# Performance work log

Measured on AMD Instinct MI355X. Metric: run time of the kernel, lower is better.

## Reference

```python
import jax, jax.numpy as jnp
import numpy as np

NUM_HEADS = 8
HEAD_DIM = 128
MAX_RES = 224.0


def rope_embed(feat_shape, dim, max_res=MAX_RES):
    # timm pixel_freq_bands: 2**linspace(0, log2(max_res)-1, dim//4) * pi
    num_bands = dim // 4
    bands = (2.0 ** jnp.linspace(0.0, float(np.log2(max_res)) - 1.0, num_bands)) * jnp.pi
    # pixel coords in [-1, 1] per spatial dim
    coords = [jnp.linspace(-1.0, 1.0, s) for s in feat_shape]
    grid = jnp.stack(jnp.meshgrid(*coords, indexing='ij'), axis=-1)[..., None]  # [H,W,2,1]
    pos = grid * bands  # [H,W,2,num_bands]
    n = int(np.prod(feat_shape))
    sin = jnp.repeat(jnp.sin(pos).reshape(n, -1), 2, axis=-1)  # [n, dim]
    cos = jnp.repeat(jnp.cos(pos).reshape(n, -1), 2, axis=-1)  # [n, dim]
    return sin, cos


def _rot(x):
    # interleaved rotate-half: (x0,x1,x2,x3,...) -> (-x1,x0,-x3,x2,...)
    return jnp.stack([-x[..., 1::2], x[..., ::2]], axis=-1).reshape(x.shape)


def setup_inputs() -> dict:
    key = jax.random.key(0)
    k1, k2, k3, k4 = jax.random.split(key, 4)
    C, E = 1024, 1024
    x = jax.random.normal(k1, (64, C, 16, 16), dtype=jnp.float32)
    qkv_w = jax.random.normal(k2, (3 * E, C), dtype=jnp.float32) * (C ** -0.5)
    qkv_b = jnp.zeros((3 * E,), dtype=jnp.float32)
    proj_w = jax.random.normal(k3, (E, E), dtype=jnp.float32) * (E ** -0.5)
    proj_b = jax.random.normal(k4, (E,), dtype=jnp.float32) * 0.02
    return {"x": x, "qkv_w": qkv_w, "qkv_b": qkv_b, "proj_w": proj_w, "proj_b": proj_b}


def reference(x, qkv_w, qkv_b, proj_w, proj_b):
    B, C, H, W = x.shape
    n = H * W
    scale = HEAD_DIM ** -0.5
    sin_emb, cos_emb = rope_embed((H, W), HEAD_DIM)  # [n, head_dim]

    t = x.reshape(B, C, n).transpose(0, 2, 1)                      # [B, n, C]
    t = jnp.concatenate([t.mean(axis=1, keepdims=True), t], axis=1)  # [B, n+1, C]

    qkv = t @ qkv_w.T + qkv_b                                      # [B, n+1, 3E]
    qkv = qkv.reshape(B, n + 1, 3, NUM_HEADS, HEAD_DIM).transpose(2, 0, 3, 1, 4)
    q, k, v = qkv[0], qkv[1], qkv[2]                               # [B, h, n+1, d]

    def apply_rope(z):
        zc, zs = z[:, :, :1], z[:, :, 1:]
        zs = zs * cos_emb + _rot(zs) * sin_emb
        return jnp.concatenate([zc, zs], axis=2)

    q = apply_rope(q)
    k = apply_rope(k)

    attn = jax.nn.softmax(jnp.einsum('bhqd,bhkd->bhqk', q, k) * scale, axis=-1)
    out = jnp.einsum('bhqk,bhkd->bhqd', attn, v)
    out = out.transpose(0, 2, 1, 3).reshape(B, n + 1, -1)           # [B, n+1, E]
    out = out @ proj_w.T + proj_b
    return out[:, 0]
```

## Files before the change

kernel.cpp:

```cpp
#include <hip/hip_runtime.h>
#include <math.h>

#define PI_F 3.14159265358979323846f
#define KSTEP 0.21959209425992272f

using bf16x8 = __attribute__((ext_vector_type(8))) short;
using f32x4 = __attribute__((ext_vector_type(4))) float;
using u16x8 = __attribute__((ext_vector_type(8))) unsigned short;

static __device__ __forceinline__ float wave_reduce_sum(float v) {
#pragma unroll
  for (int off = 32; off; off >>= 1) v += __shfl_down(v, off);
  return v;
}

static __device__ __forceinline__ unsigned short f2bf(float f) {
  unsigned u = __float_as_uint(f);
  return (unsigned short)((u + 0x7fffu + ((u >> 16) & 1u)) >> 16);
}

static __device__ __forceinline__ float bf2f(unsigned short s) {
  return __uint_as_float(((unsigned)s) << 16);
}

static __device__ __forceinline__ void gload_lds16(const void* g, void* l) {
  __builtin_amdgcn_global_load_lds((const __attribute__((address_space(1))) unsigned int*)g,
                                   (__attribute__((address_space(3))) unsigned int*)l, 16, 0, 0);
}

__global__ __launch_bounds__(256) void prep_kernel(const float* __restrict__ x,
                                                   const float* __restrict__ qkv_w,
                                                   const float* __restrict__ qkv_b,
                                                   unsigned short* __restrict__ xt,
                                                   float* __restrict__ t_mean,
                                                   unsigned short* __restrict__ wkT,
                                                   float2* __restrict__ sc) {
  const int bid = blockIdx.x;
  const int t = threadIdx.x;
  __shared__ float tile[64 * 33];
  __shared__ float tl2[64 * 65];
  if (bid < 1024) {
    const int ct = bid & 15, b = bid >> 4;
    const int cl = t >> 2, pq = (t & 3) * 8;
    const int pl = t >> 3, cq = (t & 7) * 8;
    float sum = 0.0f;
    const float* xrow = x + ((size_t)(b * 1024 + ct * 64 + cl) * 256) + pq;
    unsigned short* xtb = xt + (size_t)b * 262144 + ct * 64;
    for (int pt = 0; pt < 8; ++pt) {
      const float4 v0 = *reinterpret_cast<const float4*>(xrow + pt * 32);
      const float4 v1 = *reinterpret_cast<const float4*>(xrow + pt * 32 + 4);
      tile[cl * 33 + pq + 0] = v0.x; tile[cl * 33 + pq + 1] = v0.y;
      tile[cl * 33 + pq + 2] = v0.z; tile[cl * 33 + pq + 3] = v0.w;
      tile[cl * 33 + pq + 4] = v1.x; tile[cl * 33 + pq + 5] = v1.y;
      tile[cl * 33 + pq + 6] = v1.z; tile[cl * 33 + pq + 7] = v1.w;
      sum += (v0.x + v0.y) + (v0.z + v0.w) + (v1.x + v1.y) + (v1.z + v1.w);
      __syncthreads();
      u16x8 o;
#pragma unroll
      for (int e = 0; e < 8; ++e) o[e] = f2bf(tile[(cq + e) * 33 + pl]);
      *reinterpret_cast<u16x8*>(xtb + (size_t)(pt * 32 + pl) * 1024 + cq) = o;
      __syncthreads();
    }
    sum += __shfl_xor(sum, 1);
    sum += __shfl_xor(sum, 2);
    if ((t & 3) == 0) t_mean[b * 1024 + ct * 64 + cl] = sum * (1.0f / 256.0f);
  } else if (bid < 1280) {
    const int bb = bid - 1024;
    const int h = bb >> 5, t5 = bb & 31;
    const int dt = t5 >> 4, ct = t5 & 15;
    {
      const int dl = t >> 2, cq = (t & 3) * 16;
      const float* src = qkv_w + (size_t)(1024 + h * 128 + dt * 64 + dl) * 1024 + ct * 64 + cq;
#pragma unroll
      for (int i = 0; i < 4; ++i) {
        const float4 v = *reinterpret_cast<const float4*>(src + i * 4);
        tl2[dl * 65 + cq + i * 4 + 0] = v.x; tl2[dl * 65 + cq + i * 4 + 1] = v.y;
        tl2[dl * 65 + cq + i * 4 + 2] = v.z; tl2[dl * 65 + cq + i * 4 + 3] = v.w;
      }
    }
    __syncthreads();
    {
      const int cl = t >> 2, dq = (t & 3) * 16;
      unsigned short* dst = wkT + (size_t)(h * 1152 + ct * 64 + cl) * 128 + dt * 64 + dq;
      u16x8 o0, o1;
#pragma unroll
      for (int e = 0; e < 8; ++e) {
        o0[e] = f2bf(tl2[(dq + e) * 65 + cl]);
        o1[e] = f2bf(tl2[(dq + 8 + e) * 65 + cl]);
      }
      *reinterpret_cast<u16x8*>(dst) = o0;
      *reinterpret_cast<u16x8*>(dst + 8) = o1;
    }
  } else if (bid < 1288) {
    const int h = bid - 1280;
    for (int idx = t; idx < 16384; idx += 256) {
      const int row = 1024 + (idx >> 7), d = idx & 127;
      unsigned short v = 0;
      if (row == 1024) v = f2bf(qkv_b[1024 + h * 128 + d]);
      wkT[(size_t)(h * 1152 + row) * 128 + d] = v;
    }
  } else {
    const int idx = (bid - 1288) * 256 + t;
    const int m = idx >> 8, j = idx & 255;
    const float band = exp2f((float)(m & 31) * KSTEP) * PI_F;
    const float coord = (m < 32) ? (-1.0f + (2.0f / 15.0f) * (float)(j >> 4))
                                 : (-1.0f + (2.0f / 15.0f) * (float)(j & 15));
    float sn, cs;
    sincosf(coord * band, &sn, &cs);
    sc[idx] = make_float2(sn, cs);
  }
}

__global__ __launch_bounds__(256) void gemm_splitk(
    const float* __restrict__ A, int lda, int aStrideZ,
    const float* __restrict__ B, int ldb, int bStrideZ,
    float* __restrict__ Cp, int ldc, int cStrideZ, int cStrideKc, int KC) {
  const int nt = blockIdx.x, mt = blockIdx.y;
  const int z = blockIdx.z / KC, kc = blockIdx.z % KC;
  const int tid = threadIdx.x;
  A += (size_t)z * aStrideZ + (size_t)mt * 32 * lda + kc * 256;
  B += (size_t)z * bStrideZ + (size_t)nt * 64 * ldb + kc * 256;
  Cp += (size_t)kc * cStrideKc + (size_t)z * cStrideZ + (size_t)mt * 32 * ldc + nt * 64;

  __shared__ float As[32][34];
  __shared__ float Bs[32][68];

  const int tm = tid >> 4;
  const int tn = tid & 15;
  float acc0[4] = {0, 0, 0, 0}, acc1[4] = {0, 0, 0, 0};

  for (int k0 = 0; k0 < 256; k0 += 32) {
    {
      const int m = tid >> 3, kq = tid & 7;
      float4 v = *reinterpret_cast<const float4*>(A + (size_t)m * lda + k0 + kq * 4);
      As[kq * 4 + 0][m] = v.x; As[kq * 4 + 1][m] = v.y;
      As[kq * 4 + 2][m] = v.z; As[kq * 4 + 3][m] = v.w;
    }
#pragma unroll
    for (int r = 0; r < 2; ++r) {
      const int idx = r * 256 + tid;
      const int n = idx >> 3, kq = idx & 7;
      float4 v = *reinterpret_cast<const float4*>(B + (size_t)n * ldb + k0 + kq * 4);
      Bs[kq * 4 + 0][n] = v.x; Bs[kq * 4 + 1][n] = v.y;
      Bs[kq * 4 + 2][n] = v.z; Bs[kq * 4 + 3][n] = v.w;
    }
    __syncthreads();
#pragma unroll
    for (int k = 0; k < 32; ++k) {
      const float a0 = As[k][tm * 2], a1 = As[k][tm * 2 + 1];
      const float4 bb = *reinterpret_cast<const float4*>(&Bs[k][tn * 4]);
      acc0[0] += a0 * bb.x; acc0[1] += a0 * bb.y; acc0[2] += a0 * bb.z; acc0[3] += a0 * bb.w;
      acc1[0] += a1 * bb.x; acc1[1] += a1 * bb.y; acc1[2] += a1 * bb.z; acc1[3] += a1 * bb.w;
    }
    __syncthreads();
  }
  *reinterpret_cast<float4*>(Cp + (size_t)(tm * 2) * ldc + tn * 4) =
      make_float4(acc0[0], acc0[1], acc0[2], acc0[3]);
  *reinterpret_cast<float4*>(Cp + (size_t)(tm * 2 + 1) * ldc + tn * 4) =
      make_float4(acc1[0], acc1[1], acc1[2], acc1[3]);
}

__global__ __launch_bounds__(256) void gemm_proj_splitk(
    const float* __restrict__ Apart, const float* __restrict__ abias,
    const float* __restrict__ B, float* __restrict__ Cp) {
  const int nt = blockIdx.x, mt = blockIdx.y, kc = blockIdx.z;
  const int tid = threadIdx.x;
  B += (size_t)nt * 64 * 1024 + kc * 256;
  Cp += (size_t)kc * 65536 + (size_t)mt * 32 * 1024 + nt * 64;

  __shared__ float As[32][34];
  __shared__ float Bs[32][68];

  const int tm = tid >> 4;
  const int tn = tid & 15;
  float acc0[4] = {0, 0, 0, 0}, acc1[4] = {0, 0, 0, 0};

  for (int k0 = 0; k0 < 256; k0 += 32) {
    {
      const int m = tid >> 3, kq = tid & 7;
      const int kg = kc * 256 + k0 + kq * 4;
      const float* Ab = Apart + (size_t)(mt * 32 + m) * 1024 + kg;
      float4 v = *reinterpret_cast<const float4*>(abias + kg);
#pragma unroll
      for (int r = 0; r < 4; ++r) {
        const float4 p = *reinterpret_cast<const float4*>(Ab + (size_t)r * 65536);
        v.x += p.x; v.y += p.y; v.z += p.z; v.w += p.w;
      }
      As[kq * 4 + 0][m] = v.x; As[kq * 4 + 1][m] = v.y;
      As[kq * 4 + 2][m] = v.z; As[kq * 4 + 3][m] = v.w;
    }
#pragma unroll
    for (int r = 0; r < 2; ++r) {
      const int idx = r * 256 + tid;
      const int n = idx >> 3, kq = idx & 7;
      float4 v = *reinterpret_cast<const float4*>(B + (size_t)n * 1024 + k0 + kq * 4);
      Bs[kq * 4 + 0][n] = v.x; Bs[kq * 4 + 1][n] = v.y;
      Bs[kq * 4 + 2][n] = v.z; Bs[kq * 4 + 3][n] = v.w;
    }
    __syncthreads();
#pragma unroll
    for (int k = 0; k < 32; ++k) {
      const float a0 = As[k][tm * 2], a1 = As[k][tm * 2 + 1];
      const float4 bb = *reinterpret_cast<const float4*>(&Bs[k][tn * 4]);
      acc0[0] += a0 * bb.x; acc0[1] += a0 * bb.y; acc0[2] += a0 * bb.z; acc0[3] += a0 * bb.w;
      acc1[0] += a1 * bb.x; acc1[1] += a1 * bb.y; acc1[2] += a1 * bb.z; acc1[3] += a1 * bb.w;
    }
    __syncthreads();
  }
  *reinterpret_cast<float4*>(Cp + (size_t)(tm * 2) * 1024 + tn * 4) =
      make_float4(acc0[0], acc0[1], acc0[2], acc0[3]);
  *reinterpret_cast<float4*>(Cp + (size_t)(tm * 2 + 1) * 1024 + tn * 4) =
      make_float4(acc1[0], acc1[1], acc1[2], acc1[3]);
}

__global__ __launch_bounds__(256) void reduce4_bias(const float* __restrict__ part,
                                                    const float* __restrict__ bias,
                                                    float* __restrict__ out) {
  const int i = blockIdx.x * 256 + threadIdx.x;
  out[i] = part[i] + part[i + 65536] + part[i + 131072] + part[i + 196608] + bias[i & 1023];
}

__global__ __launch_bounds__(256) void tgemm_rot(
    const unsigned short* __restrict__ wkT, const float* __restrict__ q0p,
    const float* __restrict__ qkv_b, const float2* __restrict__ sc,
    unsigned short* __restrict__ T) {
  const int nt = blockIdx.x;
  const int mt = blockIdx.y;
  const int z = blockIdx.z;
  const int h = z >> 1, s = z & 1;
  const int tid = threadIdx.x;
  const int w = tid >> 6, lane = tid & 63;
  const int wr = w >> 1, wc = w & 1;

  __shared__ __align__(16) char smem[34816];
  char* Ab = smem;
  char* Bb = smem + 16384;
  float* q0red = reinterpret_cast<float*>(smem + 32768);

#pragma unroll
  for (int i = 0; i < 4; ++i) {
    const int g = w * 4 + i;
    const int row = g * 8 + (lane >> 3);
    const int sl = ((lane & 7) ^ ((row >> 1) & 7)) * 8;
    gload_lds16(wkT + ((size_t)h * 1152 + nt * 128 + row) * 128 + s * 64 + sl, Bb + g * 1024);
  }
  for (int idx = tid; idx < 512; idx += 256) {
    const int bl = idx >> 6, d = idx & 63;
    const int b = mt * 8 + bl;
    const float* qp = q0p + (size_t)b * 2048 + h * 128 + s * 64 + d;
    q0red[idx] = qkv_b[h * 128 + s * 64 + d] + qp[0] + qp[131072] + qp[262144] + qp[393216];
  }
  __syncthreads();

  {
    const int r = tid >> 1;
    const int ph = (tid & 1) * 16;
    const int v = r & 15;
    const int jrep = (s == 0) ? v * 16 : v;
    const float* qr = q0red + (r >> 4) * 64;
    const int swz = (r >> 1) & 7;
#pragma unroll
    for (int g = 0; g < 4; ++g) {
      unsigned pk[4];
#pragma unroll
      for (int e = 0; e < 4; ++e) {
        const int p = ph + g * 4 + e;
        const float qe = qr[2 * p], qo = qr[2 * p + 1];
        const float2 tt = sc[(s * 32 + p) * 256 + jrep];
        const float ae = qe * tt.y + qo * tt.x;
        const float ao = qo * tt.y - qe * tt.x;
        pk[e] = (unsigned)f2bf(ae) | ((unsigned)f2bf(ao) << 16);
      }
      const int slot = ((ph >> 2) + g) ^ swz;
      *reinterpret_cast<uint4*>(Ab + r * 128 + slot * 16) = make_uint4(pk[0], pk[1], pk[2], pk[3]);
    }
  }
  __syncthreads();

  f32x4 acc[4][4] = {};
#pragma unroll
  for (int kk = 0; kk < 2; ++kk) {
    bf16x8 af[4], bf[4];
#pragma unroll
    for (int mi = 0; mi < 4; ++mi) {
      const int row = wr * 64 + mi * 16 + (lane & 15);
      const int slot = (kk * 4 + (lane >> 4)) ^ ((row >> 1) & 7);
      af[mi] = *reinterpret_cast<const bf16x8*>(Ab + row * 128 + (slot << 4));
    }
#pragma unroll
    for (int ni = 0; ni < 4; ++ni) {
      const int row = wc * 64 + ni * 16 + (lane & 15);
      const int slot = (kk * 4 + (lane >> 4)) ^ ((row >> 1) & 7);
      bf[ni] = *reinterpret_cast<const bf16x8*>(Bb + row * 128 + (slot << 4));
    }
#pragma unroll
    for (int mi = 0; mi < 4; ++mi)
#pragma unroll
      for (int ni = 0; ni < 4; ++ni)
        acc[mi][ni] = __builtin_amdgcn_mfma_f32_16x16x32_bf16(af[mi], bf[ni], acc[mi][ni], 0, 0, 0);
  }

  unsigned short* Tz = T + (size_t)(s * 8 + h) * 1024 * 1152;
#pragma unroll
  for (int mi = 0; mi < 4; ++mi)
#pragma unroll
    for (int ni = 0; ni < 4; ++ni) {
      const int col = nt * 128 + wc * 64 + ni * 16 + (lane & 15);
#pragma unroll
      for (int rr = 0; rr < 4; ++rr) {
        const int row = mt * 128 + wr * 64 + mi * 16 + (lane >> 4) * 4 + rr;
        Tz[(size_t)row * 1152 + col] = f2bf(acc[mi][ni][rr]);
      }
    }
}

__global__ __launch_bounds__(512, 1) void scores_u(
    const unsigned short* __restrict__ Tg, const unsigned short* __restrict__ xt,
    const float* __restrict__ q0p, const float* __restrict__ qkv_b,
    const float* __restrict__ t_mean, float* __restrict__ u) {
  const int l = blockIdx.x;
  const int b = ((l >> 5) << 3) | (l & 7);
  const int ht = (l >> 3) & 3;
  const int tid = threadIdx.x;
  const int w = tid >> 6, lane = tid & 63;

  __shared__ __align__(16) char smem[122880];

  const unsigned short* xtb = xt + (size_t)b * 262144;

#define STAGE(buf, c0)                                                          \
  {                                                                             \
    char* Ab_ = smem + (buf)*40960;                                             \
    char* Bb_ = Ab_ + 32768;                                                    \
    _Pragma("unroll") for (int i = 0; i < 4; ++i) {                             \
      const int row_ = w * 32 + i * 8 + (lane >> 3);                            \
      const int sl_ = ((lane & 7) ^ ((row_ >> 1) & 7)) * 8;                     \
      gload_lds16(xtb + (size_t)row_ * 1024 + (c0) + sl_,                       \
                  Ab_ + (w * 4 + i) * 1024);                                    \
    }                                                                           \
    {                                                                           \
      const int n_ = w * 8 + (lane >> 3);                                       \
      const int h_ = ht * 2 + (n_ >> 5), s_ = (n_ >> 4) & 1, v_ = n_ & 15;      \
      const size_t rowT_ = ((size_t)(s_ * 8 + h_) * 1024 + b * 16 + v_) * 1152; \
      const int sl_ = ((lane & 7) ^ ((n_ >> 1) & 7)) * 8;                       \
      gload_lds16(Tg + rowT_ + (c0) + sl_, Bb_ + w * 1024);                     \
    }                                                                           \
  }

  STAGE(0, 0);
  STAGE(1, 64);
  f32x4 acc[2][4] = {};
  for (int t = 0; t < 16; ++t) {
    {
      const int src = (t + 2 > 15) ? 15 : (t + 2);
      STAGE((t + 2) % 3, src * 64);
    }
    asm volatile("s_waitcnt vmcnt(10)" ::: "memory");
    __builtin_amdgcn_s_barrier();
    const char* Ab = smem + (t % 3) * 40960;
    const char* Bb = Ab + 32768;
#pragma unroll
    for (int kk = 0; kk < 2; ++kk) {
      bf16x8 af[2], bfr[4];
#pragma unroll
      for (int mi = 0; mi < 2; ++mi) {
        const int row = w * 32 + mi * 16 + (lane & 15);
        const int slot = (kk * 4 + (lane >> 4)) ^ ((row >> 1) & 7);
        af[mi] = *reinterpret_cast<const bf16x8*>(Ab + row * 128 + (slot << 4));
      }
#pragma unroll
      for (int ni = 0; ni < 4; ++ni) {
        const int n = ni * 16 + (lane & 15);
        const int slot = (kk * 4 + (lane >> 4)) ^ ((n >> 1) & 7);
        bfr[ni] = *reinterpret_cast<const bf16x8*>(Bb + n * 128 + (slot << 4));
      }
      __builtin_amdgcn_s_setprio(1);
#pragma unroll
      for (int mi = 0; mi < 2; ++mi)
#pragma unroll
        for (int ni = 0; ni < 4; ++ni)
          acc[mi][ni] =
              __builtin_amdgcn_mfma_f32_16x16x32_bf16(af[mi], bfr[ni], acc[mi][ni], 0, 0, 0);
      __builtin_amdgcn_s_setprio(0);
    }
    __builtin_amdgcn_s_barrier();
    asm volatile("" ::: "memory");
  }
#undef STAGE

  asm volatile("s_waitcnt vmcnt(0)" ::: "memory");
  __syncthreads();

  float* Sp = reinterpret_cast<float*>(smem);
  float* bias = Sp + 1024;
  float* q0l = bias + 64;
  float* k0l = q0l + 256;
  float* ps = k0l + 256;
  float* smax = ps + 4;
  float* ssum = smax + 8;
  float* attnl = ssum + 8;
  float* upart = reinterpret_cast<float*>(smem + 16384);

#pragma unroll
  for (int mi = 0; mi < 2; ++mi)
#pragma unroll
    for (int ni = 0; ni < 4; ++ni)
#pragma unroll
      for (int rr = 0; rr < 4; ++rr) {
        const int j = w * 32 + mi * 16 + ((lane >> 4) << 2) + rr;
        const int col = ni * 16 + (lane & 15);
        const int s = (col >> 4) & 1;
        const int sel = s ? (j & 15) : (j >> 4);
        if ((col & 15) == sel) Sp[(j * 2 + (col >> 5)) * 2 + s] = acc[mi][ni][rr];
      }
  if (tid < 64) {
    const int h_ = tid >> 5, s_ = (tid >> 4) & 1, v_ = tid & 15;
    bias[tid] =
        bf2f(Tg[((size_t)(s_ * 8 + ht * 2 + h_) * 1024 + b * 16 + v_) * 1152 + 1024]);
  }
  if (tid < 256) {
    const float* qp = q0p + (size_t)b * 2048 + ht * 256 + tid;
    q0l[tid] = qkv_b[ht * 256 + tid] + qp[0] + qp[131072] + qp[262144] + qp[393216];
    const float* kp = qp + 1024;
    k0l[tid] = qkv_b[1024 + ht * 256 + tid] + kp[0] + kp[131072] + kp[262144] + kp[393216];
  }
  __syncthreads();
  if (tid < 256) {
    float pr = q0l[tid] * k0l[tid];
    pr = wave_reduce_sum(pr);
    if (lane == 0) ps[w] = pr;
  }
  __syncthreads();

  const float scale = 0.08838834764831845f;
  float e0 = 0.0f, e1 = 0.0f, eb0 = 0.0f, eb1 = 0.0f;
  if (tid < 256) {
    const float va0 = scale * (Sp[tid * 4 + 0] + Sp[tid * 4 + 1] + bias[tid >> 4] +
                               bias[16 + (tid & 15)]);
    const float va1 = scale * (Sp[tid * 4 + 2] + Sp[tid * 4 + 3] + bias[32 + (tid >> 4)] +
                               bias[48 + (tid & 15)]);
    float vb0 = -3.0e38f, vb1 = -3.0e38f;
    if (tid == 0) {
      vb0 = scale * (ps[0] + ps[1]);
      vb1 = scale * (ps[2] + ps[3]);
    }
    float m0 = fmaxf(va0, vb0), m1 = fmaxf(va1, vb1);
#pragma unroll
    for (int off = 32; off; off >>= 1) {
      m0 = fmaxf(m0, __shfl_xor(m0, off));
      m1 = fmaxf(m1, __shfl_xor(m1, off));
    }
    if (lane == 0) { smax[w] = m0; smax[4 + w] = m1; }
  }
  __syncthreads();
  if (tid < 256) {
    const float g0 = fmaxf(fmaxf(smax[0], smax[1]), fmaxf(smax[2], smax[3]));
    const float g1 = fmaxf(fmaxf(smax[4], smax[5]), fmaxf(smax[6], smax[7]));
    const float va0 = scale * (Sp[tid * 4 + 0] + Sp[tid * 4 + 1] + bias[tid >> 4] +
                               bias[16 + (tid & 15)]);
    const float va1 = scale * (Sp[tid * 4 + 2] + Sp[tid * 4 + 3] + bias[32 + (tid >> 4)] +
                               bias[48 + (tid & 15)]);
    e0 = expf(va0 - g0);
    e1 = expf(va1 - g1);
    if (tid == 0) {
      eb0 = expf(scale * (ps[0] + ps[1]) - g0);
      eb1 = expf(scale * (ps[2] + ps[3]) - g1);
    }
    float s0 = e0 + eb0, s1 = e1 + eb1;
#pragma unroll
    for (int off = 32; off; off >>= 1) {
      s0 += __shfl_xor(s0, off);
      s1 += __shfl_xor(s1, off);
    }
    if (lane == 0) { ssum[w] = s0; ssum[4 + w] = s1; }
  }
  __syncthreads();
  if (tid < 256) {
    const float inv0 = 1.0f / (ssum[0] + ssum[1] + ssum[2] + ssum[3]);
    const float inv1 = 1.0f / (ssum[4] + ssum[5] + ssum[6] + ssum[7]);
    attnl[1 + tid] = e0 * inv0;
    attnl[257 + 1 + tid] = e1 * inv1;
    if (tid == 0) { attnl[0] = eb0 * inv0; attnl[257] = eb1 * inv1; }
  }
  __syncthreads();

  {
    float ua0[16] = {}, ua1[16] = {};
    const unsigned short* xr = xtb + (size_t)(w * 32) * 1024 + lane * 16;
    for (int jj = 0; jj < 32; ++jj) {
      const float a0 = attnl[1 + w * 32 + jj];
      const float a1 = attnl[257 + 1 + w * 32 + jj];
      const u16x8 v0 = *reinterpret_cast<const u16x8*>(xr + (size_t)jj * 1024);
      const u16x8 v1 = *reinterpret_cast<const u16x8*>(xr + (size_t)jj * 1024 + 8);
#pragma unroll
      for (int e = 0; e < 8; ++e) {
        const float f0 = bf2f((unsigned short)v0[e]);
        const float f1 = bf2f((unsigned short)v1[e]);
        ua0[e] += a0 * f0; ua0[8 + e] += a0 * f1;
        ua1[e] += a1 * f0; ua1[8 + e] += a1 * f1;
      }
    }
#pragma unroll
    for (int e = 0; e < 16; ++e) {
      upart[(w * 2 + 0) * 1024 + lane * 16 + e] = ua0[e];
      upart[(w * 2 + 1) * 1024 + lane * 16 + e] = ua1[e];
    }
  }
  __syncthreads();
#pragma unroll
  for (int r = 0; r < 4; ++r) {
    const int o = tid * 4 + r;
    const int h2 = o >> 10, c = o & 1023;
    float s = 0.0f;
#pragma unroll
    for (int ww = 0; ww < 8; ++ww) s += upart[(ww * 2 + h2) * 1024 + c];
    s += attnl[h2 * 257] * t_mean[b * 1024 + c];
    u[((size_t)b * 8 + ht * 2 + h2) * 1024 + c] = s;
  }
}

extern "C" void kernel_launch(void* const* d_in, const int* in_sizes, int n_in,
                              void* d_out, int out_size, void* d_ws, size_t ws_size,
                              hipStream_t stream) {
  const float* x = (const float*)d_in[0];
  const float* qkv_w = (const float*)d_in[1];
  const float* qkv_b = (const float*)d_in[2];
  const float* proj_w = (const float*)d_in[3];
  const float* proj_b = (const float*)d_in[4];
  float* out = (float*)d_out;

  float* ws = (float*)d_ws;
  float* t_mean = ws;
  float* q0k0_part = ws + 65536;
  float* u = ws + 589824;
  float* out0_part = ws + 1114112;
  float* out_part = ws + 1376256;
  float2* sc = (float2*)(ws + 1638400);
  unsigned short* wkT = (unsigned short*)(ws + 1671168);
  unsigned short* T = (unsigned short*)(ws + 2260992);
  unsigned short* x_t = (unsigned short*)(ws + 11698176);

  prep_kernel<<<1352, 256, 0, stream>>>(x, qkv_w, qkv_b, x_t, t_mean, wkT, sc);

  gemm_splitk<<<dim3(32, 2, 4), 256, 0, stream>>>(t_mean, 1024, 0, qkv_w, 1024, 0,
                                                  q0k0_part, 2048, 0, 131072, 4);

  tgemm_rot<<<dim3(9, 8, 16), 256, 0, stream>>>(wkT, q0k0_part, qkv_b, sc, T);

  scores_u<<<256, 512, 0, stream>>>(T, x_t, q0k0_part, qkv_b, t_mean, u);

  gemm_splitk<<<dim3(2, 2, 32), 256, 0, stream>>>(u, 8192, 1024,
                                                  qkv_w + (size_t)2048 * 1024, 1024, 131072,
                                                  out0_part, 1024, 128, 65536, 4);

  gemm_proj_splitk<<<dim3(16, 2, 4), 256, 0, stream>>>(out0_part, qkv_b + 2048, proj_w, out_part);

  reduce4_bias<<<256, 256, 0, stream>>>(out_part, proj_b, out);
}
```

Baseline: 100.2 us.

## Fuse rotated-query/key-weight GEMM into scores kernel, dropping T intermediate

Removes the tgemm_rot kernel that materialized a large bf16 T buffer (rotated query times key weights) in global memory. scores_u now builds the rotated query fragments in registers, computes each 64-column T slice on the fly with MFMA from staged wkT tiles, and feeds it through LDS into the existing score GEMM. The key-bias term is computed directly instead of being read from a padded wkT row. This saves one launch and a large global write/read round trip. The cost is extra MFMA work and barriers per K-step, and the pipeline drops from triple to double buffering.

```diff
diff --git a/kernel.cpp b/kernel.cpp
--- a/kernel.cpp
+++ b/kernel.cpp
@@ -91,16 +91,8 @@
       *reinterpret_cast<u16x8*>(dst) = o0;
       *reinterpret_cast<u16x8*>(dst + 8) = o1;
     }
-  } else if (bid < 1288) {
-    const int h = bid - 1280;
-    for (int idx = t; idx < 16384; idx += 256) {
-      const int row = 1024 + (idx >> 7), d = idx & 127;
-      unsigned short v = 0;
-      if (row == 1024) v = f2bf(qkv_b[1024 + h * 128 + d]);
-      wkT[(size_t)(h * 1152 + row) * 128 + d] = v;
-    }
   } else {
-    const int idx = (bid - 1288) * 256 + t;
+    const int idx = (bid - 1280) * 256 + t;
     const int m = idx >> 8, j = idx & 255;
     const float band = exp2f((float)(m & 31) * KSTEP) * PI_F;
     const float coord = (m < 32) ? (-1.0f + (2.0f / 15.0f) * (float)(j >> 4))
@@ -220,204 +212,60 @@
   out[i] = part[i] + part[i + 65536] + part[i + 131072] + part[i + 196608] + bias[i & 1023];
 }
 
-__global__ __launch_bounds__(256) void tgemm_rot(
-    const unsigned short* __restrict__ wkT, const float* __restrict__ q0p,
-    const float* __restrict__ qkv_b, const float2* __restrict__ sc,
-    unsigned short* __restrict__ T) {
-  const int nt = blockIdx.x;
-  const int mt = blockIdx.y;
-  const int z = blockIdx.z;
-  const int h = z >> 1, s = z & 1;
-  const int tid = threadIdx.x;
-  const int w = tid >> 6, lane = tid & 63;
-  const int wr = w >> 1, wc = w & 1;
-
-  __shared__ __align__(16) char smem[34816];
-  char* Ab = smem;
-  char* Bb = smem + 16384;
-  float* q0red = reinterpret_cast<float*>(smem + 32768);
-
-#pragma unroll
-  for (int i = 0; i < 4; ++i) {
-    const int g = w * 4 + i;
-    const int row = g * 8 + (lane >> 3);
-    const int sl = ((lane & 7) ^ ((row >> 1) & 7)) * 8;
-    gload_lds16(wkT + ((size_t)h * 1152 + nt * 128 + row) * 128 + s * 64 + sl, Bb + g * 1024);
-  }
-  for (int idx = tid; idx < 512; idx += 256) {
-    const int bl = idx >> 6, d = idx & 63;
-    const int b = mt * 8 + bl;
-    const float* qp = q0p + (size_t)b * 2048 + h * 128 + s * 64 + d;
-    q0red[idx] = qkv_b[h * 128 + s * 64 + d] + qp[0] + qp[131072] + qp[262144] + qp[393216];
-  }
-  __syncthreads();
-
-  {
-    const int r = tid >> 1;
-    const int ph = (tid & 1) * 16;
-    const int v = r & 15;
-    const int jrep = (s == 0) ? v * 16 : v;
-    const float* qr = q0red + (r >> 4) * 64;
-    const int swz = (r >> 1) & 7;
-#pragma unroll
-    for (int g = 0; g < 4; ++g) {
-      unsigned pk[4];
-#pragma unroll
-      for (int e = 0; e < 4; ++e) {
-        const int p = ph + g * 4 + e;
-        const float qe = qr[2 * p], qo = qr[2 * p + 1];
-        const float2 tt = sc[(s * 32 + p) * 256 + jrep];
-        const float ae = qe * tt.y + qo * tt.x;
-        const float ao = qo * tt.y - qe * tt.x;
-        pk[e] = (unsigned)f2bf(ae) | ((unsigned)f2bf(ao) << 16);
-      }
-      const int slot = ((ph >> 2) + g) ^ swz;
-      *reinterpret_cast<uint4*>(Ab + r * 128 + slot * 16) = make_uint4(pk[0], pk[1], pk[2], pk[3]);
-    }
-  }
-  __syncthreads();
-
-  f32x4 acc[4][4] = {};
-#pragma unroll
-  for (int kk = 0; kk < 2; ++kk) {
-    bf16x8 af[4], bf[4];
-#pragma unroll
-    for (int mi = 0; mi < 4; ++mi) {
-      const int row = wr * 64 + mi * 16 + (lane & 15);
-      const int slot = (kk * 4 + (lane >> 4)) ^ ((row >> 1) & 7);
-      af[mi] = *reinterpret_cast<const bf16x8*>(Ab + row * 128 + (slot << 4));
-    }
-#pragma unroll
-    for (int ni = 0; ni < 4; ++ni) {
-      const int row = wc * 64 + ni * 16 + (lane & 15);
-      const int slot = (kk * 4 + (lane >> 4)) ^ ((row >> 1) & 7);
-      bf[ni] = *reinterpret_cast<const bf16x8*>(Bb + row * 128 + (slot << 4));
-    }
-#pragma unroll
-    for (int mi = 0; mi < 4; ++mi)
-#pragma unroll
-      for (int ni = 0; ni < 4; ++ni)
-        acc[mi][ni] = __builtin_amdgcn_mfma_f32_16x16x32_bf16(af[mi], bf[ni], acc[mi][ni], 0, 0, 0);
-  }
-
-  unsigned short* Tz = T + (size_t)(s * 8 + h) * 1024 * 1152;
-#pragma unroll
-  for (int mi = 0; mi < 4; ++mi)
-#pragma unroll
-    for (int ni = 0; ni < 4; ++ni) {
-      const int col = nt * 128 + wc * 64 + ni * 16 + (lane & 15);
-#pragma unroll
-      for (int rr = 0; rr < 4; ++rr) {
-        const int row = mt * 128 + wr * 64 + mi * 16 + (lane >> 4) * 4 + rr;
-        Tz[(size_t)row * 1152 + col] = f2bf(acc[mi][ni][rr]);
-      }
-    }
-}
-
 __global__ __launch_bounds__(512, 1) void scores_u(
-    const unsigned short* __restrict__ Tg, const unsigned short* __restrict__ xt,
+    const unsigned short* __restrict__ wkT, const unsigned short* __restrict__ xt,
     const float* __restrict__ q0p, const float* __restrict__ qkv_b,
-    const float* __restrict__ t_mean, float* __restrict__ u) {
+    const float2* __restrict__ sc, const float* __restrict__ t_mean,
+    float* __restrict__ u) {
   const int l = blockIdx.x;
   const int b = ((l >> 5) << 3) | (l & 7);
   const int ht = (l >> 3) & 3;
   const int tid = threadIdx.x;
   const int w = tid >> 6, lane = tid & 63;
-
-  __shared__ __align__(16) char smem[122880];
+  const int rgrp = lane >> 4;
+
+  const int hh_ = w >> 2, sgen = (w >> 1) & 1, ch = w & 1;
+  const int kap = hh_ * 2 + sgen;
+
+  __shared__ __align__(16) char smem[143872];
+  float* persist = reinterpret_cast<float*>(smem + 139264);
+  float* q0l = persist;
+  float* k0l = persist + 256;
+  float* biasg = persist + 512;
+  float* ps = persist + 576;
+  float* smax = persist + 580;
+  float* ssum = persist + 588;
+  float* attnl = persist + 596;
+  char* Btile = smem + 131072;
 
   const unsigned short* xtb = xt + (size_t)b * 262144;
 
-#define STAGE(buf, c0)                                                          \
+#define STAGE_A(buf, c0)                                                        \
   {                                                                             \
-    char* Ab_ = smem + (buf)*40960;                                             \
-    char* Bb_ = Ab_ + 32768;                                                    \
+    char* Ab_ = smem + (buf)*32768;                                             \
     _Pragma("unroll") for (int i = 0; i < 4; ++i) {                             \
       const int row_ = w * 32 + i * 8 + (lane >> 3);                            \
       const int sl_ = ((lane & 7) ^ ((row_ >> 1) & 7)) * 8;                     \
       gload_lds16(xtb + (size_t)row_ * 1024 + (c0) + sl_,                       \
                   Ab_ + (w * 4 + i) * 1024);                                    \
     }                                                                           \
-    {                                                                           \
-      const int n_ = w * 8 + (lane >> 3);                                       \
-      const int h_ = ht * 2 + (n_ >> 5), s_ = (n_ >> 4) & 1, v_ = n_ & 15;      \
-      const size_t rowT_ = ((size_t)(s_ * 8 + h_) * 1024 + b * 16 + v_) * 1152; \
-      const int sl_ = ((lane & 7) ^ ((n_ >> 1) & 7)) * 8;                       \
-      gload_lds16(Tg + rowT_ + (c0) + sl_, Bb_ + w * 1024);                     \
+  }
+#define STAGE_W(buf, c0)                                                        \
+  {                                                                             \
+    char* Wb_ = smem + 65536 + (buf)*32768;                                     \
+    _Pragma("unroll") for (int i = 0; i < 4; ++i) {                             \
+      const int r_ = w * 16 + i * 4 + (lane >> 4);                  \
+      const int c_ = r_ & 63;                                                   \
+      const int L_ = lane & 15;                                                 \
+      const int so_ = (L_ >> 3) * 64 + ((L_ & 7) ^ ((c_ >> 1) & 7)) * 8;        \
+      gload_lds16(wkT + ((size_t)(ht * 2 + (r_ >> 6)) * 1152 + (c0) + c_) * 128 \
+                      + so_,                                                    \
+                  Wb_ + (w * 16 + i * 4) * 256);                                \
     }                                                                           \
   }
 
-  STAGE(0, 0);
-  STAGE(1, 64);
-  f32x4 acc[2][4] = {};
-  for (int t = 0; t < 16; ++t) {
-    {
-      const int src = (t + 2 > 15) ? 15 : (t + 2);
-      STAGE((t + 2) % 3, src * 64);
-    }
-    asm volatile("s_waitcnt vmcnt(10)" ::: "memory");
-    __builtin_amdgcn_s_barrier();
-    const char* Ab = smem + (t % 3) * 40960;
-    const char* Bb = Ab + 32768;
-#pragma unroll
-    for (int kk = 0; kk < 2; ++kk) {
-      bf16x8 af[2], bfr[4];
-#pragma unroll
-      for (int mi = 0; mi < 2; ++mi) {
-        const int row = w * 32 + mi * 16 + (lane & 15);
-        const int slot = (kk * 4 + (lane >> 4)) ^ ((row >> 1) & 7);
-        af[mi] = *reinterpret_cast<const bf16x8*>(Ab + row * 128 + (slot << 4));
-      }
-#pragma unroll
-      for (int ni = 0; ni < 4; ++ni) {
-        const int n = ni * 16 + (lane & 15);
-        const int slot = (kk * 4 + (lane >> 4)) ^ ((n >> 1) & 7);
-        bfr[ni] = *reinterpret_cast<const bf16x8*>(Bb + n * 128 + (slot << 4));
-      }
-      __builtin_amdgcn_s_setprio(1);
-#pragma unroll
-      for (int mi = 0; mi < 2; ++mi)
-#pragma unroll
-        for (int ni = 0; ni < 4; ++ni)
-          acc[mi][ni] =
-              __builtin_amdgcn_mfma_f32_16x16x32_bf16(af[mi], bfr[ni], acc[mi][ni], 0, 0, 0);
-      __builtin_amdgcn_s_setprio(0);
-    }
-    __builtin_amdgcn_s_barrier();
-    asm volatile("" ::: "memory");
-  }
-#undef STAGE
-
-  asm volatile("s_waitcnt vmcnt(0)" ::: "memory");
-  __syncthreads();
-
-  float* Sp = reinterpret_cast<float*>(smem);
-  float* bias = Sp + 1024;
-  float* q0l = bias + 64;
-  float* k0l = q0l + 256;
-  float* ps = k0l + 256;
-  float* smax = ps + 4;
-  float* ssum = smax + 8;
-  float* attnl = ssum + 8;
-  float* upart = reinterpret_cast<float*>(smem + 16384);
-
-#pragma unroll
-  for (int mi = 0; mi < 2; ++mi)
-#pragma unroll
-    for (int ni = 0; ni < 4; ++ni)
-#pragma unroll
-      for (int rr = 0; rr < 4; ++rr) {
-        const int j = w * 32 + mi * 16 + ((lane >> 4) << 2) + rr;
-        const int col = ni * 16 + (lane & 15);
-        const int s = (col >> 4) & 1;
-        const int sel = s ? (j & 15) : (j >> 4);
-        if ((col & 15) == sel) Sp[(j * 2 + (col >> 5)) * 2 + s] = acc[mi][ni][rr];
-      }
-  if (tid < 64) {
-    const int h_ = tid >> 5, s_ = (tid >> 4) & 1, v_ = tid & 15;
-    bias[tid] =
-        bf2f(Tg[((size_t)(s_ * 8 + ht * 2 + h_) * 1024 + b * 16 + v_) * 1152 + 1024]);
-  }
+  STAGE_A(0, 0);
+  STAGE_W(0, 0);
   if (tid < 256) {
     const float* qp = q0p + (size_t)b * 2048 + ht * 256 + tid;
     q0l[tid] = qkv_b[ht * 256 + tid] + qp[0] + qp[131072] + qp[262144] + qp[393216];
@@ -425,6 +273,124 @@
     k0l[tid] = qkv_b[1024 + ht * 256 + tid] + kp[0] + kp[131072] + kp[262144] + kp[393216];
   }
   __syncthreads();
+
+  bf16x8 rq[2];
+  {
+    const int v = lane & 15;
+    const int jrep = sgen ? v : v * 16;
+#pragma unroll
+    for (int kk = 0; kk < 2; ++kk) {
+#pragma unroll
+      for (int e = 0; e < 8; e += 2) {
+        const int d = kk * 32 + rgrp * 8 + e;
+        const int p = d >> 1;
+        const float qe = q0l[hh_ * 128 + sgen * 64 + 2 * p];
+        const float qo = q0l[hh_ * 128 + sgen * 64 + 2 * p + 1];
+        const float2 tt = sc[(sgen * 32 + p) * 256 + jrep];
+        rq[kk][e] = (short)f2bf(qe * tt.y + qo * tt.x);
+        rq[kk][e + 1] = (short)f2bf(qo * tt.y - qe * tt.x);
+      }
+    }
+  }
+
+  f32x4 acc[2][4] = {};
+  for (int t = 0; t < 16; ++t) {
+    {
+      const int src = (t + 1 > 15) ? 15 : (t + 1);
+      STAGE_A((t + 1) & 1, src * 64);
+      STAGE_W((t + 1) & 1, src * 64);
+    }
+    asm volatile("s_waitcnt vmcnt(8)" ::: "memory");
+    __builtin_amdgcn_s_barrier();
+    const char* Ab = smem + (t & 1) * 32768;
+    const char* Wb = smem + 65536 + (t & 1) * 32768;
+    {
+      f32x4 accg[2] = {};
+#pragma unroll
+      for (int kk = 0; kk < 2; ++kk) {
+#pragma unroll
+        for (int mt = 0; mt < 2; ++mt) {
+          const int c_ = ch * 32 + mt * 16 + (lane & 15);
+          const int slot = sgen * 8 + (((kk * 4 + rgrp)) ^ ((c_ >> 1) & 7));
+          const bf16x8 wf = *reinterpret_cast<const bf16x8*>(
+              Wb + (hh_ * 64 + c_) * 256 + (slot << 4));
+          accg[mt] = __builtin_amdgcn_mfma_f32_16x16x32_bf16(wf, rq[kk], accg[mt], 0, 0, 0);
+        }
+      }
+#pragma unroll
+      for (int mt = 0; mt < 2; ++mt) {
+        const int cl = ch * 32 + mt * 16 + rgrp * 4;
+        const int n = kap * 16 + (lane & 15);
+        const unsigned u0 = (unsigned)f2bf(accg[mt][0]) | ((unsigned)f2bf(accg[mt][1]) << 16);
+        const unsigned u1 = (unsigned)f2bf(accg[mt][2]) | ((unsigned)f2bf(accg[mt][3]) << 16);
+        *reinterpret_cast<uint2*>(Btile + n * 128 + ((((cl >> 3) ^ ((n >> 1) & 7))) << 4) +
+                                  (rgrp & 1) * 8) = make_uint2(u0, u1);
+      }
+    }
+    asm volatile("s_waitcnt lgkmcnt(0)" ::: "memory");
+    __builtin_amdgcn_s_barrier();
+#pragma unroll
+    for (int kk = 0; kk < 2; ++kk) {
+      bf16x8 af[2], bfr[4];
+#pragma unroll
+      for (int mi = 0; mi < 2; ++mi) {
+        const int row = w * 32 + mi * 16 + (lane & 15);
+        const int slot = (kk * 4 + rgrp) ^ ((row >> 1) & 7);
+        af[mi] = *reinterpret_cast<const bf16x8*>(Ab + row * 128 + (slot << 4));
+      }
+#pragma unroll
+      for (int ni = 0; ni < 4; ++ni) {
+        const int n = ni * 16 + (lane & 15);
+        const int slot = (kk * 4 + rgrp) ^ ((n >> 1) & 7);
+        bfr[ni] = *reinterpret_cast<const bf16x8*>(Btile + n * 128 + (slot << 4));
+      }
+      __builtin_amdgcn_s_setprio(1);
+#pragma unroll
+      for (int mi = 0; mi < 2; ++mi)
+#pragma unroll
+        for (int ni = 0; ni < 4; ++ni)
+          acc[mi][ni] =
+              __builtin_amdgcn_mfma_f32_16x16x32_bf16(af[mi], bfr[ni], acc[mi][ni], 0, 0, 0);
+      __builtin_amdgcn_s_setprio(0);
+    }
+    __builtin_amdgcn_s_barrier();
+    asm volatile("" ::: "memory");
+  }
+#undef STAGE_A
+#undef STAGE_W
+
+  asm volatile("s_waitcnt vmcnt(0)" ::: "memory");
+  __syncthreads();
+
+  float* Sp = reinterpret_cast<float*>(smem);
+  float* upart = reinterpret_cast<float*>(smem + 16384);
+
+#pragma unroll
+  for (int mi = 0; mi < 2; ++mi)
+#pragma unroll
+    for (int ni = 0; ni < 4; ++ni)
+#pragma unroll
+      for (int rr = 0; rr < 4; ++rr) {
+        const int j = w * 32 + mi * 16 + (rgrp << 2) + rr;
+        const int col = ni * 16 + (lane & 15);
+        const int s = (col >> 4) & 1;
+        const int sel = s ? (j & 15) : (j >> 4);
+        if ((col & 15) == sel) Sp[(j * 2 + (col >> 5)) * 2 + s] = acc[mi][ni][rr];
+      }
+  if (tid < 64) {
+    const int h_ = tid >> 5, s_ = (tid >> 4) & 1, v_ = tid & 15;
+    const float* bk = qkv_b + 1024 + (ht * 2 + h_) * 128 + s_ * 64;
+    const int jrep = s_ ? v_ : v_ * 16;
+    float a = 0.0f;
+#pragma unroll 4
+    for (int p = 0; p < 32; ++p) {
+      const float qe = q0l[h_ * 128 + s_ * 64 + 2 * p];
+      const float qo = q0l[h_ * 128 + s_ * 64 + 2 * p + 1];
+      const float2 tt = sc[(s_ * 32 + p) * 256 + jrep];
+      a += (qe * tt.y + qo * tt.x) * bk[2 * p] + (qo * tt.y - qe * tt.x) * bk[2 * p + 1];
+    }
+    biasg[tid] = a;
+  }
   if (tid < 256) {
     float pr = q0l[tid] * k0l[tid];
     pr = wave_reduce_sum(pr);
@@ -435,10 +401,10 @@
   const float scale = 0.08838834764831845f;
   float e0 = 0.0f, e1 = 0.0f, eb0 = 0.0f, eb1 = 0.0f;
   if (tid < 256) {
-    const float va0 = scale * (Sp[tid * 4 + 0] + Sp[tid * 4 + 1] + bias[tid >> 4] +
-                               bias[16 + (tid & 15)]);
-    const float va1 = scale * (Sp[tid * 4 + 2] + Sp[tid * 4 + 3] + bias[32 + (tid >> 4)] +
-                               bias[48 + (tid & 15)]);
+    const float va0 = scale * (Sp[tid * 4 + 0] + Sp[tid * 4 + 1] + biasg[tid >> 4] +
+                               biasg[16 + (tid & 15)]);
+    const float va1 = scale * (Sp[tid * 4 + 2] + Sp[tid * 4 + 3] + biasg[32 + (tid >> 4)] +
+                               biasg[48 + (tid & 15)]);
     float vb0 = -3.0e38f, vb1 = -3.0e38f;
     if (tid == 0) {
       vb0 = scale * (ps[0] + ps[1]);
@@ -456,10 +422,10 @@
   if (tid < 256) {
     const float g0 = fmaxf(fmaxf(smax[0], smax[1]), fmaxf(smax[2], smax[3]));
     const float g1 = fmaxf(fmaxf(smax[4], smax[5]), fmaxf(smax[6], smax[7]));
-    const float va0 = scale * (Sp[tid * 4 + 0] + Sp[tid * 4 + 1] + bias[tid >> 4] +
-                               bias[16 + (tid & 15)]);
-    const float va1 = scale * (Sp[tid * 4 + 2] + Sp[tid * 4 + 3] + bias[32 + (tid >> 4)] +
-                               bias[48 + (tid & 15)]);
+    const float va0 = scale * (Sp[tid * 4 + 0] + Sp[tid * 4 + 1] + biasg[tid >> 4] +
+                               biasg[16 + (tid & 15)]);
+    const float va1 = scale * (Sp[tid * 4 + 2] + Sp[tid * 4 + 3] + biasg[32 + (tid >> 4)] +
+                               biasg[48 + (tid & 15)]);
     e0 = expf(va0 - g0);
     e1 = expf(va1 - g1);
     if (tid == 0) {
@@ -537,17 +503,14 @@
   float* out_part = ws + 1376256;
   float2* sc = (float2*)(ws + 1638400);
   unsigned short* wkT = (unsigned short*)(ws + 1671168);
-  unsigned short* T = (unsigned short*)(ws + 2260992);
   unsigned short* x_t = (unsigned short*)(ws + 11698176);
 
-  prep_kernel<<<1352, 256, 0, stream>>>(x, qkv_w, qkv_b, x_t, t_mean, wkT, sc);
+  prep_kernel<<<1344, 256, 0, stream>>>(x, qkv_w, qkv_b, x_t, t_mean, wkT, sc);
 
   gemm_splitk<<<dim3(32, 2, 4), 256, 0, stream>>>(t_mean, 1024, 0, qkv_w, 1024, 0,
                                                   q0k0_part, 2048, 0, 131072, 4);
 
-  tgemm_rot<<<dim3(9, 8, 16), 256, 0, stream>>>(wkT, q0k0_part, qkv_b, sc, T);
-
-  scores_u<<<256, 512, 0, stream>>>(T, x_t, q0k0_part, qkv_b, t_mean, u);
+  scores_u<<<256, 512, 0, stream>>>(wkT, x_t, q0k0_part, qkv_b, sc, t_mean, u);
 
   gemm_splitk<<<dim3(2, 2, 32), 256, 0, stream>>>(u, 8192, 1024,
                                                   qkv_w + (size_t)2048 * 1024, 1024, 131072,
```

Result: faster. 95.71 us (median of 4 runs) (-4.5%).
